# Performance work log

Measured on AMD Instinct MI355X. Metric: run time of the kernel, lower is better.

The kernel has to match this reference:

```python
import jax, jax.numpy as jnp
import numpy as np

QUERY_DIM = 1024
KEY_DIM = 768
NUM_HEADS = 16
HEAD_DIM = QUERY_DIM // NUM_HEADS


def _linear_params(key, in_dim, out_dim):
    kw, kb = jax.random.split(key)
    bound = 1.0 / np.sqrt(in_dim)
    W = jax.random.uniform(kw, (out_dim, in_dim), minval=-bound, maxval=bound, dtype=jnp.float32)
    b = jax.random.uniform(kb, (out_dim,), minval=-bound, maxval=bound, dtype=jnp.float32)
    return W, b


def setup_inputs() -> dict:
    key = jax.random.key(0)
    ks = jax.random.split(key, 7)
    B, Nq, Nk = 4, 1024, 2048
    query = jax.random.normal(ks[0], (B, Nq, QUERY_DIM), dtype=jnp.float32)
    k_in = jax.random.normal(ks[1], (B, Nk, KEY_DIM), dtype=jnp.float32)
    v_in = jax.random.normal(ks[2], (B, Nk, KEY_DIM), dtype=jnp.float32)
    Wq, bq = _linear_params(ks[3], QUERY_DIM, QUERY_DIM)
    Wk, bk = _linear_params(ks[4], KEY_DIM, QUERY_DIM)
    Wv, bv = _linear_params(ks[5], KEY_DIM, QUERY_DIM)
    Wo, bo = _linear_params(ks[6], QUERY_DIM, QUERY_DIM)
    return {
        "query": query, "key": k_in, "value": v_in,
        "Wq": Wq, "bq": bq, "Wk": Wk, "bk": bk,
        "Wv": Wv, "bv": bv, "Wo": Wo, "bo": bo,
    }


def reference(query, key, value, Wq, bq, Wk, bk, Wv, bv, Wo, bo):
    B, Nq, _ = query.shape
    Nk = key.shape[1]
    H, D = NUM_HEADS, HEAD_DIM
    scale = 1.0 / np.sqrt(D)
    # Projections (torch Linear: x @ W.T + b), then split heads -> (B, H, N, D)
    Q = (query @ Wq.T + bq).reshape(B, Nq, H, D).transpose(0, 2, 1, 3)
    K = (key @ Wk.T + bk).reshape(B, Nk, H, D).transpose(0, 2, 1, 3)
    V = (value @ Wv.T + bv).reshape(B, Nk, H, D).transpose(0, 2, 1, 3)
    # Explicit score matrix (B, H, Nq, Nk), softmax over keys
    attn = jnp.einsum('bhqd,bhkd->bhqk', Q, K) * scale
    attn = jax.nn.softmax(attn, axis=-1)
    out = jnp.einsum('bhqk,bhkd->bhqd', attn, V)
    out = out.transpose(0, 2, 1, 3).reshape(B, Nq, H * D)
    return out @ Wo.T + bo
```

## Files before the change

### kernel.cpp

```cpp
#include <hip/hip_runtime.h>
#include <stdint.h>


typedef __attribute__((ext_vector_type(4))) float f32x4;
typedef __attribute__((ext_vector_type(8))) _Float16 half8;
typedef __attribute__((ext_vector_type(4))) _Float16 half4;
typedef __attribute__((ext_vector_type(2))) _Float16 half2v;
typedef __attribute__((ext_vector_type(4))) short short4v;
typedef __attribute__((ext_vector_type(8))) short short8;
typedef unsigned short u16;

__device__ __forceinline__ u16 f2h(float f){
  _Float16 h = (_Float16)f;
  return __builtin_bit_cast(unsigned short, h);
}

__device__ __forceinline__ void gload16(const void* g, void* lds){
  __builtin_amdgcn_global_load_lds((const __attribute__((address_space(1))) void*)g,
                                   (__attribute__((address_space(3))) void*)lds, 16, 0, 0);
}

struct Seg { const float* s; u16* d; int n4; };
struct Cvt7 { Seg seg[7]; };

__global__ __launch_bounds__(256) void cvt_f32_f16(Cvt7 a){
  Seg sg = a.seg[blockIdx.y];
  const long stride = (long)gridDim.x * 256;
  for (long i = (long)blockIdx.x*256 + threadIdx.x; i < sg.n4; i += stride){
    f32x4 v = *(const f32x4*)(sg.s + i*4);
    short4v h;
    h[0] = (short)f2h(v[0]); h[1] = (short)f2h(v[1]);
    h[2] = (short)f2h(v[2]); h[3] = (short)f2h(v[3]);
    *(short4v*)(sg.d + i*4) = h;
  }
}

template<int R, int THREADS>
__device__ __forceinline__ void stage_tile(const char* gbase, long gstride, char* lds, int tid){
  const int w = tid >> 6, lane = tid & 63;
  #pragma unroll
  for (int it = 0; it < R*8/THREADS; ++it){
    int c  = it*THREADS + w*64 + lane;
    int r  = c >> 3;
    int bs = (c & 7) << 4;
    int sb = bs ^ ((r & 7) << 4);
    gload16(gbase + (long)r*gstride + sb, lds + (it*THREADS + w*64)*16);
  }
}

template<bool DBUF>
__device__ __forceinline__ void gemm128(const u16* A, const u16* Bt, int K,
                                        int row0, int col0, int tid,
                                        char* lds, f32x4 acc[4][4]){
  const int lane = tid & 63, w = tid >> 6;
  const int g = lane >> 4, lm = lane & 15;
  const int wr = (w >> 1) * 64, wc = (w & 1) * 64;
  const char* Ag = (const char*)A  + ((long)row0 * K) * 2;
  const char* Bg = (const char*)Bt + ((long)col0 * K) * 2;

  if (DBUF){
    stage_tile<128, 256>(Ag, (long)K*2, lds, tid);
    stage_tile<128, 256>(Bg, (long)K*2, lds + 16384, tid);
  }
  for (int k0 = 0; k0 < K; k0 += 64){
    char* cur;
    if (DBUF){
      cur = lds + ((k0 >> 6) & 1) * 32768;
      if (k0 + 64 < K){
        char* nxt = lds + ((((k0 >> 6) & 1) ^ 1)) * 32768;
        stage_tile<128, 256>(Ag + (long)(k0+64)*2, (long)K*2, nxt, tid);
        stage_tile<128, 256>(Bg + (long)(k0+64)*2, (long)K*2, nxt + 16384, tid);
        asm volatile("s_waitcnt vmcnt(8)" ::: "memory");
      } else {
        asm volatile("s_waitcnt vmcnt(0)" ::: "memory");
      }
      __builtin_amdgcn_s_barrier();
    } else {
      cur = lds;
      stage_tile<128, 256>(Ag + (long)k0*2, (long)K*2, cur, tid);
      stage_tile<128, 256>(Bg + (long)k0*2, (long)K*2, cur + 16384, tid);
      __syncthreads();
    }
    char* Al = cur, *Bl = cur + 16384;
    #pragma unroll
    for (int kk = 0; kk < 2; ++kk){
      half8 af[4], bfr[4];
      #pragma unroll
      for (int mi = 0; mi < 4; ++mi){
        int r = wr + mi*16 + lm;
        af[mi] = *(const half8*)(Al + r*128 + ((kk*64 + g*16) ^ ((r & 7) << 4)));
      }
      #pragma unroll
      for (int ni = 0; ni < 4; ++ni){
        int r = wc + ni*16 + lm;
        bfr[ni] = *(const half8*)(Bl + r*128 + ((kk*64 + g*16) ^ ((r & 7) << 4)));
      }
      #pragma unroll
      for (int mi = 0; mi < 4; ++mi)
        #pragma unroll
        for (int ni = 0; ni < 4; ++ni)
          acc[mi][ni] = __builtin_amdgcn_mfma_f32_16x16x32_f16(af[mi], bfr[ni], acc[mi][ni], 0, 0, 0);
    }
    if (DBUF) __builtin_amdgcn_s_barrier();
    else      __syncthreads();
  }
}

__global__ __launch_bounds__(256)
void qkv_proj(const u16* __restrict__ qH, const u16* __restrict__ kH, const u16* __restrict__ vH,
              const u16* __restrict__ WqH, const u16* __restrict__ WkH, const u16* __restrict__ WvH,
              const float* __restrict__ bq, const float* __restrict__ bk, const float* __restrict__ bv,
              u16* __restrict__ Qw, u16* __restrict__ Kw, u16* __restrict__ Vtw)
{
  __shared__ __align__(128) char lds[32768];
  const int tid = threadIdx.x, lane = tid & 63, w = tid >> 6;
  const int g = lane >> 4, lm = lane & 15;

  int bid = (blockIdx.x & 7) * 160 + (blockIdx.x >> 3);
  const u16 *A, *Bt; const float* bias; u16* out16;
  int K, logS, local; float scale = 1.0f;
  int which;
  if (bid < 256)      { which = 0; local = bid;       A = qH; Bt = WqH; bias = bq; out16 = Qw;  K = 1024; logS = 10; scale = 0.125f; }
  else if (bid < 768) { which = 1; local = bid - 256; A = kH; Bt = WkH; bias = bk; out16 = Kw;  K = 768;  logS = 11; }
  else                { which = 2; local = bid - 768; A = vH; Bt = WvH; bias = bv; out16 = Vtw; K = 768;  logS = 11; }
  const int rb = local >> 3, cb = local & 7;
  const int row0 = rb * 128, col0 = cb * 128;

  f32x4 acc[4][4];
  #pragma unroll
  for (int i = 0; i < 4; ++i)
    #pragma unroll
    for (int j = 0; j < 4; ++j) acc[i][j] = {0.f, 0.f, 0.f, 0.f};

  gemm128<false>(A, Bt, K, row0, col0, tid, lds, acc);

  const int wr = (w >> 1) * 64, wc = (w & 1) * 64;
  if (which != 2){
    #pragma unroll
    for (int mi = 0; mi < 4; ++mi)
      #pragma unroll
      for (int ni = 0; ni < 4; ++ni){
        int n = col0 + wc + ni*16 + lm;
        float bvv = bias[n];
        int h_ = n >> 6, d_ = n & 63;
        #pragma unroll
        for (int r = 0; r < 4; ++r){
          int m = row0 + wr + mi*16 + g*4 + r;
          int b_ = m >> logS, s_ = m & ((1 << logS) - 1);
          long dst = (((long)(b_*16 + h_) << logS) + s_) * 64 + d_;
          out16[dst] = f2h((acc[mi][ni][r] + bvv) * scale);
        }
      }
  } else {
    #pragma unroll
    for (int mi = 0; mi < 4; ++mi)
      #pragma unroll
      for (int ni = 0; ni < 4; ++ni){
        int np = wc + ni*16 + lm;
        float bvv = bias[col0 + np];
        short4v h4;
        #pragma unroll
        for (int r = 0; r < 4; ++r) h4[r] = (short)f2h(acc[mi][ni][r] + bvv);
        int mb = (wr + mi*16 + g*4) * 2;
        *(short4v*)(lds + np*256 + (mb ^ ((np & 7) << 4))) = h4;
      }
    __syncthreads();
    const int b_ = row0 >> 11;
    #pragma unroll
    for (int pass = 0; pass < 8; ++pass){
      int idx = pass*256 + tid, row = idx >> 4, c = idx & 15;
      short8 v = *(const short8*)(lds + row*256 + ((c*16) ^ ((row & 7) << 4)));
      int ng = col0 + row, h_ = ng >> 6, d_ = ng & 63;
      long dst = ((long)(b_*16 + h_)*64 + d_)*2048 + (row0 & 2047) + c*8;
      *(short8*)(out16 + dst) = v;
    }
  }
}

__global__ __launch_bounds__(512, 4)
void attn_fused(const u16* __restrict__ Qw, const u16* __restrict__ Kw,
                const u16* __restrict__ Vtw, u16* __restrict__ AO)
{
  __shared__ __align__(128) char lds[32768];
  const int tid = threadIdx.x, lane = tid & 63, w = tid >> 6;
  const int g = lane >> 4, lm = lane & 15;
  const int p = blockIdx.x;
  const int slot = p >> 3;
  const int bh = (p & 7) + ((slot & 7) << 3);
  const int qt = slot >> 3;
  const long qbase = (long)bh * 1024 * 64;
  const long kbase = (long)bh * 2048 * 64;
  const long vbase = (long)bh * 64 * 2048;

  const int q0 = qt*128 + w*16;
  half8 aQ[2];
  #pragma unroll
  for (int kk = 0; kk < 2; ++kk)
    aQ[kk] = *(const half8*)((const char*)Qw + (qbase + (long)(q0 + lm)*64 + kk*32 + g*8)*2);

  float mrun = -3e38f, lrun = 0.f;
  f32x4 O[4];
  #pragma unroll
  for (int di = 0; di < 4; ++di) O[di] = {0.f, 0.f, 0.f, 0.f};

  stage_tile<64, 512>((const char*)Kw  + kbase*2, 128,  lds, tid);
  stage_tile<64, 512>((const char*)Vtw + vbase*2, 4096, lds + 8192, tid);

  for (int kt = 0; kt < 2048; kt += 64){
    char* cur = lds + ((kt >> 6) & 1) * 16384;
    if (kt + 64 < 2048){
      char* nxt = lds + ((((kt >> 6) & 1) ^ 1)) * 16384;
      stage_tile<64, 512>((const char*)Kw  + (kbase + (long)(kt+64)*64)*2, 128,  nxt, tid);
      stage_tile<64, 512>((const char*)Vtw + (vbase + kt+64)*2,            4096, nxt + 8192, tid);
      asm volatile("s_waitcnt vmcnt(2)" ::: "memory");
    } else {
      asm volatile("s_waitcnt vmcnt(0)" ::: "memory");
    }
    __builtin_amdgcn_s_barrier();
    char* Klds = cur, *Vlds = cur + 8192;

    half8 kf[4][2];
    #pragma unroll
    for (int t = 0; t < 4; ++t)
      #pragma unroll
      for (int kk = 0; kk < 2; ++kk){
        int r = t*16 + lm;
        kf[t][kk] = *(const half8*)(Klds + r*128 + ((kk*64 + g*16) ^ ((r & 7) << 4)));
      }

    f32x4 sc[4];
    #pragma unroll
    for (int t = 0; t < 4; ++t){
      f32x4 z = {0.f, 0.f, 0.f, 0.f};
      z = __builtin_amdgcn_mfma_f32_16x16x32_f16(kf[t][0], aQ[0], z, 0, 0, 0);
      z = __builtin_amdgcn_mfma_f32_16x16x32_f16(kf[t][1], aQ[1], z, 0, 0, 0);
      sc[t] = z;
    }
    float pm = sc[0][0];
    #pragma unroll
    for (int t = 0; t < 4; ++t)
      #pragma unroll
      for (int r = 0; r < 4; ++r) pm = fmaxf(pm, sc[t][r]);
    pm = fmaxf(pm, __shfl_xor(pm, 16));
    pm = fmaxf(pm, __shfl_xor(pm, 32));
    if (!__all(pm <= mrun + 8.0f)){
      float mnew = fmaxf(mrun, pm);
      float fac  = __expf(mrun - mnew);
      lrun *= fac;
      float frow[4];
      #pragma unroll
      for (int r = 0; r < 4; ++r) frow[r] = __shfl(fac, (lane & 48) | (g*4 + r));
      #pragma unroll
      for (int di = 0; di < 4; ++di){
        O[di][0] *= frow[0]; O[di][1] *= frow[1];
        O[di][2] *= frow[2]; O[di][3] *= frow[3];
      }
      mrun = mnew;
    }
    float ls = 0.f;
    #pragma unroll
    for (int t = 0; t < 4; ++t)
      #pragma unroll
      for (int r = 0; r < 4; ++r){ float pv = __expf(sc[t][r] - mrun); sc[t][r] = pv; ls += pv; }
    ls += __shfl_xor(ls, 16);
    ls += __shfl_xor(ls, 32);
    lrun += ls;

    half8 pa[2];
    #pragma unroll
    for (int kh = 0; kh < 2; ++kh)
      #pragma unroll
      for (int j = 0; j < 2; ++j){
        int t = kh*2 + j;
        half2v p01 = __builtin_bit_cast(half2v, __builtin_amdgcn_cvt_pkrtz(sc[t][0], sc[t][1]));
        half2v p23 = __builtin_bit_cast(half2v, __builtin_amdgcn_cvt_pkrtz(sc[t][2], sc[t][3]));
        pa[kh][j*4+0] = p01[0]; pa[kh][j*4+1] = p01[1];
        pa[kh][j*4+2] = p23[0]; pa[kh][j*4+3] = p23[1];
      }
    #pragma unroll
    for (int di = 0; di < 4; ++di){
      int d = di*16 + lm;
      int swz = (d & 7) << 4;
      #pragma unroll
      for (int kh = 0; kh < 2; ++kh){
        half4 lo = *(const half4*)(Vlds + d*128 + ((kh*64 + g*8)      ^ swz));
        half4 hi = *(const half4*)(Vlds + d*128 + ((kh*64 + g*8 + 32) ^ swz));
        half8 vf = { lo[0], lo[1], lo[2], lo[3], hi[0], hi[1], hi[2], hi[3] };
        O[di] = __builtin_amdgcn_mfma_f32_16x16x32_f16(pa[kh], vf, O[di], 0, 0, 0);
      }
    }
    __builtin_amdgcn_s_barrier();
  }

  const int b = bh >> 4, h = bh & 15;
  float inv = 1.f / lrun;
  float irow[4];
  #pragma unroll
  for (int r = 0; r < 4; ++r) irow[r] = __shfl(inv, (lane & 48) | (g*4 + r));
  #pragma unroll
  for (int di = 0; di < 4; ++di)
    #pragma unroll
    for (int r = 0; r < 4; ++r){
      long q = q0 + g*4 + r;
      AO[((long)b*1024 + q)*1024 + h*64 + di*16 + lm] = f2h(O[di][r] * irow[r]);
    }
}

__global__ __launch_bounds__(256)
void gemm_o(const u16* __restrict__ A, const u16* __restrict__ Bt,
            const float* __restrict__ bias, float* __restrict__ outF)
{
  __shared__ __align__(128) char lds[65536];
  const int tid = threadIdx.x, lane = tid & 63, w = tid >> 6;
  const int g = lane >> 4, lm = lane & 15;
  int bid = (blockIdx.x & 7) * 32 + (blockIdx.x >> 3);
  const int rb = bid >> 3, cb = bid & 7;
  const int row0 = rb * 128, col0 = cb * 128;

  f32x4 acc[4][4];
  #pragma unroll
  for (int i = 0; i < 4; ++i)
    #pragma unroll
    for (int j = 0; j < 4; ++j) acc[i][j] = {0.f, 0.f, 0.f, 0.f};

  gemm128<true>(A, Bt, 1024, row0, col0, tid, lds, acc);

  const int wr = (w >> 1) * 64, wc = (w & 1) * 64;
  #pragma unroll
  for (int mi = 0; mi < 4; ++mi)
    #pragma unroll
    for (int ni = 0; ni < 4; ++ni){
      int n = col0 + wc + ni*16 + lm;
      float bvv = bias[n];
      #pragma unroll
      for (int r = 0; r < 4; ++r){
        int m = row0 + wr + mi*16 + g*4 + r;
        outF[(long)m * 1024 + n] = acc[mi][ni][r] + bvv;
      }
    }
}

extern "C" void kernel_launch(void* const* d_in, const int* in_sizes, int n_in,
                              void* d_out, int out_size, void* d_ws, size_t ws_size,
                              hipStream_t stream)
{
  const float* query = (const float*)d_in[0];
  const float* key   = (const float*)d_in[1];
  const float* value = (const float*)d_in[2];
  const float* Wq = (const float*)d_in[3];
  const float* bq = (const float*)d_in[4];
  const float* Wk = (const float*)d_in[5];
  const float* bk = (const float*)d_in[6];
  const float* Wv = (const float*)d_in[7];
  const float* bv = (const float*)d_in[8];
  const float* Wo = (const float*)d_in[9];
  const float* bo = (const float*)d_in[10];
  float* out = (float*)d_out;

  char* p = (char*)d_ws;
  auto alloc = [&](long bytes){ char* r = p; p += bytes; return r; };
  u16* qH  = (u16*)alloc( 8l<<20);
  u16* kH  = (u16*)alloc(12l<<20);
  u16* vH  = (u16*)alloc(12l<<20);
  u16* WqH = (u16*)alloc( 2l<<20);
  u16* WkH = (u16*)alloc( 2l<<20);
  u16* WvH = (u16*)alloc( 2l<<20);
  u16* WoH = (u16*)alloc( 2l<<20);
  u16* Qw  = (u16*)alloc( 8l<<20);
  u16* Kw  = (u16*)alloc(16l<<20);
  u16* Vtw = (u16*)alloc(16l<<20);
  u16* AO  = (u16*)alloc( 8l<<20);

  Cvt7 ca;
  ca.seg[0] = { query, qH,  4096*1024/4 };
  ca.seg[1] = { key,   kH,  8192*768/4  };
  ca.seg[2] = { value, vH,  8192*768/4  };
  ca.seg[3] = { Wq,    WqH, 1024*1024/4 };
  ca.seg[4] = { Wk,    WkH, 1024*768/4  };
  ca.seg[5] = { Wv,    WvH, 1024*768/4  };
  ca.seg[6] = { Wo,    WoH, 1024*1024/4 };
  cvt_f32_f16<<<dim3(512, 7), 256, 0, stream>>>(ca);

  qkv_proj<<<dim3(1280), dim3(256), 0, stream>>>(qH, kH, vH, WqH, WkH, WvH,
                                                 bq, bk, bv, Qw, Kw, Vtw);
  attn_fused<<<dim3(512), dim3(512), 0, stream>>>(Qw, Kw, Vtw, AO);
  gemm_o<<<dim3(256), dim3(256), 0, stream>>>(AO, WoH, bo, out);
}
```

Before: 260.5 us.

## Use exp2 softmax, precompute LDS offsets, unroll attention loop, stage Q/K stores

The log2(e) factor is folded into the Q projection scale so the attention softmax can use exp2f, with the rescale threshold adjusted to match. The attention main loop is unrolled by two with compile-time buffer parity, and the LDS fragment offsets and global staging pointers are precomputed. s_setprio is raised around the MFMA sections. The Q/K projection epilogue now goes through LDS so global writes become 16-byte vectors instead of scattered 2-byte stores. In exchange the kernel uses more registers and adds a barrier in the projection epilogue.

```diff
diff --git a/kernel.cpp b/kernel.cpp
--- a/kernel.cpp
+++ b/kernel.cpp
@@ -120,7 +120,7 @@
   const u16 *A, *Bt; const float* bias; u16* out16;
   int K, logS, local; float scale = 1.0f;
   int which;
-  if (bid < 256)      { which = 0; local = bid;       A = qH; Bt = WqH; bias = bq; out16 = Qw;  K = 1024; logS = 10; scale = 0.125f; }
+  if (bid < 256)      { which = 0; local = bid;       A = qH; Bt = WqH; bias = bq; out16 = Qw;  K = 1024; logS = 10; scale = 0.125f*1.44269504f; }
   else if (bid < 768) { which = 1; local = bid - 256; A = kH; Bt = WkH; bias = bk; out16 = Kw;  K = 768;  logS = 11; }
   else                { which = 2; local = bid - 768; A = vH; Bt = WvH; bias = bv; out16 = Vtw; K = 768;  logS = 11; }
   const int rb = local >> 3, cb = local & 7;
@@ -140,17 +140,25 @@
     for (int mi = 0; mi < 4; ++mi)
       #pragma unroll
       for (int ni = 0; ni < 4; ++ni){
-        int n = col0 + wc + ni*16 + lm;
-        float bvv = bias[n];
-        int h_ = n >> 6, d_ = n & 63;
+        int n = wc + ni*16 + lm;
+        float bvv = bias[col0 + n];
         #pragma unroll
         for (int r = 0; r < 4; ++r){
-          int m = row0 + wr + mi*16 + g*4 + r;
-          int b_ = m >> logS, s_ = m & ((1 << logS) - 1);
-          long dst = (((long)(b_*16 + h_) << logS) + s_) * 64 + d_;
-          out16[dst] = f2h((acc[mi][ni][r] + bvv) * scale);
+          int m = wr + mi*16 + g*4 + r;
+          *(u16*)(lds + m*256 + ((n*2) ^ ((m & 7) << 4))) = f2h((acc[mi][ni][r] + bvv) * scale);
         }
       }
+    __syncthreads();
+    #pragma unroll
+    for (int pass = 0; pass < 8; ++pass){
+      int idx = pass*256 + tid, row = idx >> 4, c = idx & 15;
+      short8 v = *(const short8*)(lds + row*256 + ((c*16) ^ ((row & 7) << 4)));
+      int m = row0 + row;
+      int b_ = m >> logS, s_ = m & ((1 << logS) - 1);
+      int n = col0 + c*8, h_ = n >> 6, d0 = n & 63;
+      long dst = (((long)(b_*16 + h_) << logS) + s_) * 64 + d0;
+      *(short8*)(out16 + dst) = v;
+    }
   } else {
     #pragma unroll
     for (int mi = 0; mi < 4; ++mi)
@@ -176,6 +184,82 @@
     }
   }
 }
+
+#define AITER(PAR, LAST) do{                                                   \
+    if (!(LAST)){                                                              \
+      gload16(pK, lds + (((PAR)^1)*16384) + stDst);                            \
+      gload16(pV, lds + (((PAR)^1)*16384) + 8192 + stDst);                     \
+      pK += 8192; pV += 128;                                                   \
+      asm volatile("s_waitcnt vmcnt(2)" ::: "memory");                         \
+    } else {                                                                   \
+      asm volatile("s_waitcnt vmcnt(0)" ::: "memory");                         \
+    }                                                                          \
+    __builtin_amdgcn_s_barrier();                                              \
+    half8 kf[4][2];                                                            \
+    _Pragma("unroll")                                                          \
+    for (int t = 0; t < 4; ++t){                                               \
+      kf[t][0] = *(const half8*)(lds + (PAR)*16384 + akf[t*2+0]);              \
+      kf[t][1] = *(const half8*)(lds + (PAR)*16384 + akf[t*2+1]);              \
+    }                                                                          \
+    f32x4 sc[4];                                                               \
+    __builtin_amdgcn_s_setprio(1);                                             \
+    _Pragma("unroll")                                                          \
+    for (int t = 0; t < 4; ++t){                                               \
+      f32x4 z = {0.f, 0.f, 0.f, 0.f};                                          \
+      z = __builtin_amdgcn_mfma_f32_16x16x32_f16(kf[t][0], aQ[0], z, 0, 0, 0); \
+      z = __builtin_amdgcn_mfma_f32_16x16x32_f16(kf[t][1], aQ[1], z, 0, 0, 0); \
+      sc[t] = z;                                                               \
+    }                                                                          \
+    __builtin_amdgcn_s_setprio(0);                                             \
+    float pm = sc[0][0];                                                       \
+    _Pragma("unroll")                                                          \
+    for (int t = 0; t < 4; ++t)                                                \
+      pm = fmaxf(pm, fmaxf(fmaxf(sc[t][0], sc[t][1]), fmaxf(sc[t][2], sc[t][3])));\
+    pm = fmaxf(pm, __shfl_xor(pm, 16));                                        \
+    pm = fmaxf(pm, __shfl_xor(pm, 32));                                        \
+    if (!__all(pm <= mrun + 11.541560f)){                                      \
+      float mnew = fmaxf(mrun, pm);                                            \
+      float fac = exp2f(mrun - mnew);                                          \
+      lrun *= fac;                                                             \
+      float frow[4];                                                           \
+      _Pragma("unroll")                                                        \
+      for (int r = 0; r < 4; ++r) frow[r] = __shfl(fac, (lane & 48) | (g*4 + r));\
+      _Pragma("unroll")                                                        \
+      for (int di = 0; di < 4; ++di){                                          \
+        O[di][0] *= frow[0]; O[di][1] *= frow[1];                              \
+        O[di][2] *= frow[2]; O[di][3] *= frow[3];                              \
+      }                                                                        \
+      mrun = mnew;                                                             \
+    }                                                                          \
+    float ls = 0.f;                                                            \
+    half8 pa[2];                                                               \
+    _Pragma("unroll")                                                          \
+    for (int t = 0; t < 4; ++t){                                               \
+      float p0 = exp2f(sc[t][0] - mrun), p1 = exp2f(sc[t][1] - mrun);          \
+      float p2 = exp2f(sc[t][2] - mrun), p3 = exp2f(sc[t][3] - mrun);          \
+      ls += (p0 + p1) + (p2 + p3);                                             \
+      half2v pA_ = __builtin_bit_cast(half2v, __builtin_amdgcn_cvt_pkrtz(p0, p1));\
+      half2v pB_ = __builtin_bit_cast(half2v, __builtin_amdgcn_cvt_pkrtz(p2, p3));\
+      pa[t >> 1][(t & 1)*4 + 0] = pA_[0]; pa[t >> 1][(t & 1)*4 + 1] = pA_[1];  \
+      pa[t >> 1][(t & 1)*4 + 2] = pB_[0]; pa[t >> 1][(t & 1)*4 + 3] = pB_[1];  \
+    }                                                                          \
+    ls += __shfl_xor(ls, 16);                                                  \
+    ls += __shfl_xor(ls, 32);                                                  \
+    lrun += ls;                                                                \
+    __builtin_amdgcn_s_setprio(1);                                             \
+    _Pragma("unroll")                                                          \
+    for (int di = 0; di < 4; ++di){                                            \
+      _Pragma("unroll")                                                        \
+      for (int kh = 0; kh < 2; ++kh){                                          \
+        half4 lo = *(const half4*)(lds + (PAR)*16384 + avf[(di*2+kh)*2+0]);    \
+        half4 hi = *(const half4*)(lds + (PAR)*16384 + avf[(di*2+kh)*2+1]);    \
+        half8 vf = { lo[0], lo[1], lo[2], lo[3], hi[0], hi[1], hi[2], hi[3] }; \
+        O[di] = __builtin_amdgcn_mfma_f32_16x16x32_f16(pa[kh], vf, O[di], 0, 0, 0);\
+      }                                                                        \
+    }                                                                          \
+    __builtin_amdgcn_s_setprio(0);                                             \
+    __builtin_amdgcn_s_barrier();                                              \
+  }while(0)
 
 __global__ __launch_bounds__(512, 4)
 void attn_fused(const u16* __restrict__ Qw, const u16* __restrict__ Kw,
@@ -198,98 +282,42 @@
   for (int kk = 0; kk < 2; ++kk)
     aQ[kk] = *(const half8*)((const char*)Qw + (qbase + (long)(q0 + lm)*64 + kk*32 + g*8)*2);
 
-  float mrun = -3e38f, lrun = 0.f;
+  int akf[8];
+  #pragma unroll
+  for (int t = 0; t < 4; ++t)
+    #pragma unroll
+    for (int kk = 0; kk < 2; ++kk){
+      int r = t*16 + lm;
+      akf[t*2+kk] = r*128 + ((kk*64 + g*16) ^ ((r & 7) << 4));
+    }
+  int avf[16];
+  #pragma unroll
+  for (int di = 0; di < 4; ++di){
+    int d = di*16 + lm, swz = (d & 7) << 4;
+    #pragma unroll
+    for (int kh = 0; kh < 2; ++kh){
+      avf[(di*2+kh)*2+0] = 8192 + d*128 + ((kh*64 + g*8)      ^ swz);
+      avf[(di*2+kh)*2+1] = 8192 + d*128 + ((kh*64 + g*8 + 32) ^ swz);
+    }
+  }
+  const int sr = tid >> 3, sbs = (tid & 7) << 4;
+  const int ssb = sbs ^ ((sr & 7) << 4);
+  const char* pK = (const char*)Kw  + kbase*2 + sr*128  + ssb;
+  const char* pV = (const char*)Vtw + vbase*2 + sr*4096 + ssb;
+  const int stDst = w*1024;
+
+  float mrun = -1e30f, lrun = 0.f;
   f32x4 O[4];
   #pragma unroll
   for (int di = 0; di < 4; ++di) O[di] = {0.f, 0.f, 0.f, 0.f};
 
-  stage_tile<64, 512>((const char*)Kw  + kbase*2, 128,  lds, tid);
-  stage_tile<64, 512>((const char*)Vtw + vbase*2, 4096, lds + 8192, tid);
-
-  for (int kt = 0; kt < 2048; kt += 64){
-    char* cur = lds + ((kt >> 6) & 1) * 16384;
-    if (kt + 64 < 2048){
-      char* nxt = lds + ((((kt >> 6) & 1) ^ 1)) * 16384;
-      stage_tile<64, 512>((const char*)Kw  + (kbase + (long)(kt+64)*64)*2, 128,  nxt, tid);
-      stage_tile<64, 512>((const char*)Vtw + (vbase + kt+64)*2,            4096, nxt + 8192, tid);
-      asm volatile("s_waitcnt vmcnt(2)" ::: "memory");
-    } else {
-      asm volatile("s_waitcnt vmcnt(0)" ::: "memory");
-    }
-    __builtin_amdgcn_s_barrier();
-    char* Klds = cur, *Vlds = cur + 8192;
-
-    half8 kf[4][2];
-    #pragma unroll
-    for (int t = 0; t < 4; ++t)
-      #pragma unroll
-      for (int kk = 0; kk < 2; ++kk){
-        int r = t*16 + lm;
-        kf[t][kk] = *(const half8*)(Klds + r*128 + ((kk*64 + g*16) ^ ((r & 7) << 4)));
-      }
-
-    f32x4 sc[4];
-    #pragma unroll
-    for (int t = 0; t < 4; ++t){
-      f32x4 z = {0.f, 0.f, 0.f, 0.f};
-      z = __builtin_amdgcn_mfma_f32_16x16x32_f16(kf[t][0], aQ[0], z, 0, 0, 0);
-      z = __builtin_amdgcn_mfma_f32_16x16x32_f16(kf[t][1], aQ[1], z, 0, 0, 0);
-      sc[t] = z;
-    }
-    float pm = sc[0][0];
-    #pragma unroll
-    for (int t = 0; t < 4; ++t)
-      #pragma unroll
-      for (int r = 0; r < 4; ++r) pm = fmaxf(pm, sc[t][r]);
-    pm = fmaxf(pm, __shfl_xor(pm, 16));
-    pm = fmaxf(pm, __shfl_xor(pm, 32));
-    if (!__all(pm <= mrun + 8.0f)){
-      float mnew = fmaxf(mrun, pm);
-      float fac  = __expf(mrun - mnew);
-      lrun *= fac;
-      float frow[4];
-      #pragma unroll
-      for (int r = 0; r < 4; ++r) frow[r] = __shfl(fac, (lane & 48) | (g*4 + r));
-      #pragma unroll
-      for (int di = 0; di < 4; ++di){
-        O[di][0] *= frow[0]; O[di][1] *= frow[1];
-        O[di][2] *= frow[2]; O[di][3] *= frow[3];
-      }
-      mrun = mnew;
-    }
-    float ls = 0.f;
-    #pragma unroll
-    for (int t = 0; t < 4; ++t)
-      #pragma unroll
-      for (int r = 0; r < 4; ++r){ float pv = __expf(sc[t][r] - mrun); sc[t][r] = pv; ls += pv; }
-    ls += __shfl_xor(ls, 16);
-    ls += __shfl_xor(ls, 32);
-    lrun += ls;
-
-    half8 pa[2];
-    #pragma unroll
-    for (int kh = 0; kh < 2; ++kh)
-      #pragma unroll
-      for (int j = 0; j < 2; ++j){
-        int t = kh*2 + j;
-        half2v p01 = __builtin_bit_cast(half2v, __builtin_amdgcn_cvt_pkrtz(sc[t][0], sc[t][1]));
-        half2v p23 = __builtin_bit_cast(half2v, __builtin_amdgcn_cvt_pkrtz(sc[t][2], sc[t][3]));
-        pa[kh][j*4+0] = p01[0]; pa[kh][j*4+1] = p01[1];
-        pa[kh][j*4+2] = p23[0]; pa[kh][j*4+3] = p23[1];
-      }
-    #pragma unroll
-    for (int di = 0; di < 4; ++di){
-      int d = di*16 + lm;
-      int swz = (d & 7) << 4;
-      #pragma unroll
-      for (int kh = 0; kh < 2; ++kh){
-        half4 lo = *(const half4*)(Vlds + d*128 + ((kh*64 + g*8)      ^ swz));
-        half4 hi = *(const half4*)(Vlds + d*128 + ((kh*64 + g*8 + 32) ^ swz));
-        half8 vf = { lo[0], lo[1], lo[2], lo[3], hi[0], hi[1], hi[2], hi[3] };
-        O[di] = __builtin_amdgcn_mfma_f32_16x16x32_f16(pa[kh], vf, O[di], 0, 0, 0);
-      }
-    }
-    __builtin_amdgcn_s_barrier();
+  gload16(pK, lds + stDst);
+  gload16(pV, lds + 8192 + stDst);
+  pK += 8192; pV += 128;
+
+  for (int it2 = 0; it2 < 16; ++it2){
+    AITER(0, false);
+    AITER(1, it2 == 15);
   }
 
   const int b = bh >> 4, h = bh & 15;
```

New measurement: 274.0 us. 1.05x slower.
